# Performance work log

Measured on AMD Instinct MI355X. Metric: run time of the kernel, lower is better.

## Reference

```python
import jax, jax.numpy as jnp
import numpy as np

INPUT = 28
HID = 64
OUT = 10


def setup_inputs() -> dict:
    key = jax.random.key(0)
    ks = jax.random.split(key, 8)
    s_ih = 1.0 / np.sqrt(HID)
    x = jax.random.normal(ks[0], (16384, 28, INPUT), dtype=jnp.float32)
    # PyTorch LSTM params: gate order (i, f, g, o), each block of size HID
    W_ih = jax.random.uniform(ks[1], (4 * HID, INPUT), jnp.float32, -s_ih, s_ih)
    W_hh = jax.random.uniform(ks[2], (4 * HID, HID), jnp.float32, -s_ih, s_ih)
    b_ih = jax.random.uniform(ks[3], (4 * HID,), jnp.float32, -s_ih, s_ih)
    b_hh = jax.random.uniform(ks[4], (4 * HID,), jnp.float32, -s_ih, s_ih)
    s_fc = 1.0 / np.sqrt(HID)
    W_fc = jax.random.uniform(ks[5], (OUT, HID), jnp.float32, -s_fc, s_fc)
    b_fc = jax.random.uniform(ks[6], (OUT,), jnp.float32, -s_fc, s_fc)
    return {"x": x, "W_ih": W_ih, "W_hh": W_hh, "b_ih": b_ih, "b_hh": b_hh,
            "W_fc": W_fc, "b_fc": b_fc}


def reference(x, W_ih, W_hh, b_ih, b_hh, W_fc, b_fc):
    B = x.shape[0]
    # Precompute input projections for all timesteps in one big GEMM: [T, B, 4H]
    x_proj = jnp.einsum('bti,gi->tbg', x, W_ih) + (b_ih + b_hh)

    def step(carry, xp_t):
        h, c = carry
        gates = xp_t + h @ W_hh.T  # [B, 4H]
        i, f, g, o = jnp.split(gates, 4, axis=-1)
        i = jax.nn.sigmoid(i)
        f = jax.nn.sigmoid(f)
        g = jnp.tanh(g)
        o = jax.nn.sigmoid(o)
        c = f * c + i * g
        h = o * jnp.tanh(c)
        return (h, c), None

    h0 = jnp.zeros((B, HID), dtype=x.dtype)
    c0 = jnp.zeros((B, HID), dtype=x.dtype)
    (h_last, _), _ = jax.lax.scan(step, (h0, c0), x_proj)
    # fc on the last timestep's hidden state (== output[:, -1, :])
    return h_last @ W_fc.T + b_fc
```

## Files before the change

kernel.cpp:

```cpp
#include <hip/hip_runtime.h>
#include <hip/hip_bf16.h>


namespace {
constexpr int B_TOT   = 16384;
constexpr int T_STEPS = 28;
constexpr int IN_DIM  = 28;
constexpr int HID     = 64;
constexpr int OUT_DIM = 10;
constexpr int ROWS    = 16;
constexpr int THREADS = 256;
constexpr int KP      = 104;
constexpr int XROW    = T_STEPS * IN_DIM;
}

typedef __attribute__((ext_vector_type(8))) short short8v;
typedef __attribute__((ext_vector_type(4))) short short4v;
typedef __attribute__((ext_vector_type(4))) float float4v;

__device__ __forceinline__ short f2bf_cold(float f) {
  union { float f; unsigned u; } v; v.f = f;
  unsigned r = v.u + 0x7FFFu + ((v.u >> 16) & 1u);
  return (short)(r >> 16);
}
__device__ __forceinline__ float bf2f(short s) {
  union { unsigned u; float f; } v; v.u = ((unsigned)(unsigned short)s) << 16;
  return v.f;
}
__device__ __forceinline__ unsigned pk2(float a, float b) {
  __hip_bfloat162 h = __float22bfloat162_rn(float2{a, b});
  union { __hip_bfloat162 h; unsigned u; } cv; cv.h = h; return cv.u;
}
__device__ __forceinline__ float sigf(float v) {
  return __builtin_amdgcn_rcpf(1.0f + __expf(-v));
}
__device__ __forceinline__ float tanh_f(float v) {
  return 2.0f * __builtin_amdgcn_rcpf(1.0f + __expf(-2.0f * v)) - 1.0f;
}

__global__ __attribute__((amdgpu_flat_work_group_size(THREADS, THREADS),
                          amdgpu_waves_per_eu(4, 4)))
void lstm_mfma7(const float* __restrict__ x, const float* __restrict__ W_ih,
                const float* __restrict__ W_hh, const float* __restrict__ b_ih,
                const float* __restrict__ b_hh, const float* __restrict__ W_fc,
                const float* __restrict__ b_fc, float* __restrict__ out) {
  __shared__ short hs[2][ROWS][KP];

  const int tid  = threadIdx.x;
  const int lane = tid & 63;
  const int w    = tid >> 6;
  const int l15  = lane & 15;
  const int q    = lane >> 4;
  const int b0   = blockIdx.x * ROWS;

  {
    const unsigned bi = blockIdx.x;
    const unsigned ph = (bi ^ (bi >> 3) ^ (bi >> 6)) & 7u;
    for (unsigned i = 0; i < ph; ++i) __builtin_amdgcn_s_sleep(2);
  }

  short8v a[4][3];
#pragma unroll
  for (int i = 0; i < 4; ++i) {
    const int mt   = 4 * w + i;
    const int m    = 16 * mt + l15;
    const int unit = m >> 2, type = m & 3;
    const int g    = type * 64 + unit;
#pragma unroll
    for (int kc = 0; kc < 3; ++kc) {
      short8v frag;
#pragma unroll
      for (int j = 0; j < 8; ++j) {
        const int k = kc * 32 + q * 8 + j;
        float v = 0.0f;
        if (k < IN_DIM)        v = W_ih[g * IN_DIM + k];
        else if (k == IN_DIM)  v = b_ih[g] + b_hh[g];
        else if (k >= 32)      v = W_hh[g * HID + (k - 32)];
        frag[j] = f2bf_cold(v);
      }
      a[i][kc] = frag;
    }
  }

  for (int idx = tid; idx < 2 * ROWS * KP; idx += THREADS) (&hs[0][0][0])[idx] = 0;
  __syncthreads();
  if (tid < 2 * ROWS) hs[tid >> 4][tid & 15][IN_DIM] = (short)0x3F80;

  const bool stager = (lane < 28);
  const int  s  = w * 28 + lane;
  const int  sr = s / 7;
  const int  sc = s - 7 * sr;
  const float* xptr = x + (size_t)(b0 + sr) * XROW + sc * 4;

  float4 xfly = {0.f, 0.f, 0.f, 0.f};
  if (stager) {
    float4 x0 = *(const float4*)xptr;
    short4v sv;
    unsigned plo = pk2(x0.x, x0.y), phi = pk2(x0.z, x0.w);
    sv[0] = (short)(plo & 0xFFFF); sv[1] = (short)(plo >> 16);
    sv[2] = (short)(phi & 0xFFFF); sv[3] = (short)(phi >> 16);
    *(short4v*)&hs[0][sr][sc * 4] = sv;
    xfly = *(const float4*)(xptr + 1 * IN_DIM);
  }
  __syncthreads();

  float c_state[4] = {0.f, 0.f, 0.f, 0.f};

  for (int t = 0; t < T_STEPS; ++t) {
    const int cur = t & 1, nxt = cur ^ 1;

    short8v bf0 = *(const short8v*)&hs[cur][l15][q * 8];
    short8v bf1 = *(const short8v*)&hs[cur][l15][32 + q * 8];
    short8v bf2 = *(const short8v*)&hs[cur][l15][64 + q * 8];

    if (stager) {
      if (t + 1 < T_STEPS) {
        short4v sv;
        unsigned plo = pk2(xfly.x, xfly.y), phi = pk2(xfly.z, xfly.w);
        sv[0] = (short)(plo & 0xFFFF); sv[1] = (short)(plo >> 16);
        sv[2] = (short)(phi & 0xFFFF); sv[3] = (short)(phi >> 16);
        *(short4v*)&hs[nxt][sr][sc * 4] = sv;
      }
      if (t + 2 < T_STEPS)
        xfly = *(const float4*)(xptr + (t + 2) * IN_DIM);
    }

    const float4v zero4 = {0.f, 0.f, 0.f, 0.f};
    float4v acc[4];
#pragma unroll
    for (int i = 0; i < 4; ++i)
      acc[i] = __builtin_amdgcn_mfma_f32_16x16x32_bf16(a[i][0], bf0, zero4, 0, 0, 0);
#pragma unroll
    for (int i = 0; i < 4; ++i)
      acc[i] = __builtin_amdgcn_mfma_f32_16x16x32_bf16(a[i][1], bf1, acc[i], 0, 0, 0);
#pragma unroll
    for (int i = 0; i < 4; ++i)
      acc[i] = __builtin_amdgcn_mfma_f32_16x16x32_bf16(a[i][2], bf2, acc[i], 0, 0, 0);

    float hv[4];
#pragma unroll
    for (int i = 0; i < 4; ++i) {
      float4v g4 = acc[i];
      float iv = sigf(g4[0]);
      float fv = sigf(g4[1]);
      float gv = tanh_f(g4[2]);
      float ov = sigf(g4[3]);
      float cn = fv * c_state[i] + iv * gv;
      c_state[i] = cn;
      hv[i] = ov * tanh_f(cn);
    }
    unsigned p01 = pk2(hv[0], hv[1]);
    unsigned p23 = pk2(hv[2], hv[3]);
    hs[nxt][l15][32 + 16 * w + 0 + q]  = (short)(p01 & 0xFFFF);
    hs[nxt][l15][32 + 16 * w + 4 + q]  = (short)(p01 >> 16);
    hs[nxt][l15][32 + 16 * w + 8 + q]  = (short)(p23 & 0xFFFF);
    hs[nxt][l15][32 + 16 * w + 12 + q] = (short)(p23 >> 16);

    __syncthreads();
  }

  if (tid < ROWS * OUT_DIM) {
    const int r = tid / OUT_DIM;
    const int o = tid - r * OUT_DIM;
    float sacc = b_fc[o];
#pragma unroll
    for (int j = 0; j < HID; ++j)
      sacc += bf2f(hs[0][r][32 + j]) * W_fc[o * HID + j];
    out[(b0 + r) * OUT_DIM + o] = sacc;
  }
}

extern "C" void kernel_launch(void* const* d_in, const int* in_sizes, int n_in,
                              void* d_out, int out_size, void* d_ws, size_t ws_size,
                              hipStream_t stream) {
  const float* x    = (const float*)d_in[0];
  const float* W_ih = (const float*)d_in[1];
  const float* W_hh = (const float*)d_in[2];
  const float* b_ih = (const float*)d_in[3];
  const float* b_hh = (const float*)d_in[4];
  const float* W_fc = (const float*)d_in[5];
  const float* b_fc = (const float*)d_in[6];
  float* out = (float*)d_out;

  dim3 grid(B_TOT / ROWS);
  dim3 block(THREADS);
  lstm_mfma7<<<grid, block, 0, stream>>>(x, W_ih, W_hh, b_ih, b_hh, W_fc, b_fc, out);
}
```

Before: 134.8 us.

## Precompute bf16 weight fragments in prep kernel and share reciprocals across gate activations

A small prep kernel now packs W_ih, W_hh and the fused bias into bf16 MFMA fragment layout in workspace, so each block loads its fragments with vector loads instead of gathering and converting scalars. The staggered s_sleep start is removed. The gate nonlinearities are rewritten so that two sigmoids share one reciprocal (i with f, and o with tanh(c)), with the cell value clamped before exponentiation. This cuts per-step transcendental work and per-block setup, at the cost of an extra kernel launch and slightly different rounding.

```diff
diff --git a/kernel.cpp b/kernel.cpp
--- a/kernel.cpp
+++ b/kernel.cpp
@@ -12,6 +12,8 @@
 constexpr int THREADS = 256;
 constexpr int KP      = 104;
 constexpr int XROW    = T_STEPS * IN_DIM;
+constexpr int NFRAG   = 16 * 3;
+constexpr int WS_ELEMS = NFRAG * 64 * 8;
 }
 
 typedef __attribute__((ext_vector_type(8))) short short8v;
@@ -31,18 +33,35 @@
   __hip_bfloat162 h = __float22bfloat162_rn(float2{a, b});
   union { __hip_bfloat162 h; unsigned u; } cv; cv.h = h; return cv.u;
 }
-__device__ __forceinline__ float sigf(float v) {
-  return __builtin_amdgcn_rcpf(1.0f + __expf(-v));
-}
-__device__ __forceinline__ float tanh_f(float v) {
-  return 2.0f * __builtin_amdgcn_rcpf(1.0f + __expf(-2.0f * v)) - 1.0f;
+
+__global__ void lstm_prep(const float* __restrict__ W_ih,
+                          const float* __restrict__ W_hh,
+                          const float* __restrict__ b_ih,
+                          const float* __restrict__ b_hh,
+                          unsigned short* __restrict__ ws) {
+  int idx = blockIdx.x * blockDim.x + threadIdx.x;
+  if (idx >= WS_ELEMS) return;
+  int j  = idx & 7;
+  int l  = (idx >> 3) & 63;
+  int fk = idx >> 9;
+  int kc = fk % 3;
+  int mt = fk / 3;
+  int m  = 16 * mt + (l & 15);
+  int unit = m >> 2, type = m & 3;
+  int g  = type * 64 + unit;
+  int k  = kc * 32 + (l >> 4) * 8 + j;
+  float v = 0.0f;
+  if (k < IN_DIM)        v = W_ih[g * IN_DIM + k];
+  else if (k == IN_DIM)  v = b_ih[g] + b_hh[g];
+  else if (k >= 32)      v = W_hh[g * HID + (k - 32)];
+  ws[idx] = (unsigned short)f2bf_cold(v);
 }
 
 __global__ __attribute__((amdgpu_flat_work_group_size(THREADS, THREADS),
                           amdgpu_waves_per_eu(4, 4)))
-void lstm_mfma7(const float* __restrict__ x, const float* __restrict__ W_ih,
-                const float* __restrict__ W_hh, const float* __restrict__ b_ih,
-                const float* __restrict__ b_hh, const float* __restrict__ W_fc,
+void lstm_mfma8(const float* __restrict__ x,
+                const unsigned short* __restrict__ wfrag,
+                const float* __restrict__ W_fc,
                 const float* __restrict__ b_fc, float* __restrict__ out) {
   __shared__ short hs[2][ROWS][KP];
 
@@ -53,34 +72,12 @@
   const int q    = lane >> 4;
   const int b0   = blockIdx.x * ROWS;
 
-  {
-    const unsigned bi = blockIdx.x;
-    const unsigned ph = (bi ^ (bi >> 3) ^ (bi >> 6)) & 7u;
-    for (unsigned i = 0; i < ph; ++i) __builtin_amdgcn_s_sleep(2);
-  }
-
   short8v a[4][3];
 #pragma unroll
-  for (int i = 0; i < 4; ++i) {
-    const int mt   = 4 * w + i;
-    const int m    = 16 * mt + l15;
-    const int unit = m >> 2, type = m & 3;
-    const int g    = type * 64 + unit;
+  for (int i = 0; i < 4; ++i)
 #pragma unroll
-    for (int kc = 0; kc < 3; ++kc) {
-      short8v frag;
-#pragma unroll
-      for (int j = 0; j < 8; ++j) {
-        const int k = kc * 32 + q * 8 + j;
-        float v = 0.0f;
-        if (k < IN_DIM)        v = W_ih[g * IN_DIM + k];
-        else if (k == IN_DIM)  v = b_ih[g] + b_hh[g];
-        else if (k >= 32)      v = W_hh[g * HID + (k - 32)];
-        frag[j] = f2bf_cold(v);
-      }
-      a[i][kc] = frag;
-    }
-  }
+    for (int kc = 0; kc < 3; ++kc)
+      a[i][kc] = *(const short8v*)&wfrag[((((4 * w + i) * 3) + kc) * 64 + lane) * 8];
 
   for (int idx = tid; idx < 2 * ROWS * KP; idx += THREADS) (&hs[0][0][0])[idx] = 0;
   __syncthreads();
@@ -141,13 +138,24 @@
 #pragma unroll
     for (int i = 0; i < 4; ++i) {
       float4v g4 = acc[i];
-      float iv = sigf(g4[0]);
-      float fv = sigf(g4[1]);
-      float gv = tanh_f(g4[2]);
-      float ov = sigf(g4[3]);
-      float cn = fv * c_state[i] + iv * gv;
+      float Ei = __expf(-g4[0]);
+      float Ef = __expf(-g4[1]);
+      float Eg = __expf(-2.0f * g4[2]);
+      float Eo = __expf(-g4[3]);
+      float di = 1.0f + Ei, df = 1.0f + Ef;
+      float r1 = __builtin_amdgcn_rcpf(di * df);
+      float iv = r1 * df;
+      float fv = r1 * di;
+      float gv = fmaf(2.0f, __builtin_amdgcn_rcpf(1.0f + Eg), -1.0f);
+      float cn = fmaf(fv, c_state[i], iv * gv);
       c_state[i] = cn;
-      hv[i] = ov * tanh_f(cn);
+      float ct = fminf(fmaxf(cn, -15.0f), 15.0f);
+      float Ec = __expf(-2.0f * ct);
+      float dn = 1.0f + Eo, dc = 1.0f + Ec;
+      float r2 = __builtin_amdgcn_rcpf(dn * dc);
+      float ov = r2 * dc;
+      float tc = fmaf(2.0f * r2, dn, -1.0f);
+      hv[i] = ov * tc;
     }
     unsigned p01 = pk2(hv[0], hv[1]);
     unsigned p23 = pk2(hv[2], hv[3]);
@@ -181,8 +189,11 @@
   const float* W_fc = (const float*)d_in[5];
   const float* b_fc = (const float*)d_in[6];
   float* out = (float*)d_out;
+  unsigned short* ws = (unsigned short*)d_ws;
+
+  lstm_prep<<<(WS_ELEMS + 255) / 256, 256, 0, stream>>>(W_ih, W_hh, b_ih, b_hh, ws);
 
   dim3 grid(B_TOT / ROWS);
   dim3 block(THREADS);
-  lstm_mfma7<<<grid, block, 0, stream>>>(x, W_ih, W_hh, b_ih, b_hh, W_fc, b_fc, out);
+  lstm_mfma8<<<grid, block, 0, stream>>>(x, ws, W_fc, b_fc, out);
 }
```

Result: no change. 132.3 us (-1.8%).
